# Performance work log

Hardware: AMD Instinct MI355X
Metric: run time of the kernel (lower is better)

Reference implementation:

```python
import jax, jax.numpy as jnp
import numpy as np

B, C, H, W = 64, 256, 32, 32
HID = C // 16          # SE hidden = channels // ratio
EMB = 16               # channel/snr embed dim
COND = 2 * EMB         # cond vector dim = 32
RHID = 64              # rate controller hidden
SNR_DB = 10.0
CH_IDX = 2             # 'Combined_channel'
POWER = 2.0
BASE_CR, MIN_CR, MAX_CR, ALPHA = 0.5, 0.3, 1.0, 0.7


def setup_inputs() -> dict:
    key = jax.random.key(0)
    ks = jax.random.split(key, 16)
    g = lambda k, sh: (jax.random.normal(k, sh, dtype=jnp.float32) * 0.05)
    return {
        "x": jax.random.normal(ks[0], (B, C, H, W), dtype=jnp.float32),
        "channel_embed": g(ks[1], (3, EMB)),
        "snr_w1": g(ks[2], (EMB, 1)), "snr_b1": jnp.zeros((EMB,), jnp.float32),
        "snr_w2": g(ks[3], (EMB, EMB)), "snr_b2": jnp.zeros((EMB,), jnp.float32),
        "base_w1": g(ks[4], (HID, C)),
        "base_w2": g(ks[5], (C, HID)),
        "sem_proj": g(ks[6], (HID, C)),
        "cond_proj": g(ks[7], (HID, COND)),
        "out_proj": g(ks[8], (C, HID)),
        "r_w1": g(ks[9], (RHID, C + COND)), "r_b1": jnp.zeros((RHID,), jnp.float32),
        "r_w2": g(ks[10], (RHID, RHID)), "r_b2": jnp.zeros((RHID,), jnp.float32),
        "r_w3": g(ks[11], (1, RHID)), "r_b3": jnp.zeros((1,), jnp.float32),
    }


def _topk_mask(weights, k):
    # weights [B,C], k [B] int; keep top-k per row (vectorized rank trick).
    order = jnp.argsort(-weights, axis=1)
    ranks = jnp.argsort(order, axis=1)
    return (ranks < k[:, None]).astype(weights.dtype)


def reference(x, channel_embed, snr_w1, snr_b1, snr_w2, snr_b2,
              base_w1, base_w2, sem_proj, cond_proj, out_proj,
              r_w1, r_b1, r_w2, r_b2, r_w3, r_b3):
    b, c, h, w = x.shape
    sem = x.mean(axis=(2, 3))                                   # [B,C] GAP
    # channel condition encoder
    ch_vec = jnp.broadcast_to(channel_embed[CH_IDX], (b, EMB))
    s_in = jnp.full((b, 1), SNR_DB / 28.0, dtype=x.dtype)
    sv = jax.nn.relu(s_in @ snr_w1.T + snr_b1)
    sv = jax.nn.relu(sv @ snr_w2.T + snr_b2)
    cond = jnp.concatenate([ch_vec, sv], axis=1)                # [B,32]
    # base SE weights * channel-conditioned gate
    base = jax.nn.sigmoid(jax.nn.relu(sem @ base_w1.T) @ base_w2.T)
    gate = jax.nn.sigmoid(jax.nn.relu(sem @ sem_proj.T + cond @ cond_proj.T) @ out_proj.T)
    weights = base * gate                                       # [B,C]
    # rate controller -> per-sample cr
    r = jax.nn.relu(jnp.concatenate([sem, cond], axis=1) @ r_w1.T + r_b1)
    r = jax.nn.relu(r @ r_w2.T + r_b2)
    raw = jax.nn.sigmoid(r @ r_w3.T + r_b3)[:, 0]
    dyn = MIN_CR + (MAX_CR - MIN_CR) * raw
    cr = jnp.clip((1.0 - ALPHA) * BASE_CR + ALPHA * dyn, MIN_CR, MAX_CR)
    k = jnp.clip(jnp.round(cr * c).astype(jnp.int32), 1, c)
    mask = _topk_mask(weights, k)
    z = x * (weights * mask)[:, :, None, None]                  # masked latent
    # --- combined channel: flat Rayleigh fading + per-(b,c,h) AWGN ---
    F = c * h * w
    zf = z.reshape(b, F)
    xr, xi = zf[:, 0::2], zf[:, 1::2]                           # [B,F/2]
    nk = jax.random.split(jax.random.key(42), 5)
    hr = jax.random.normal(nk[0], xr.shape, x.dtype)            # torch h_i (real)
    hi = jax.random.normal(nk[1], xr.shape, x.dtype)            # torch h_r (imag)
    std = jnp.sqrt(jnp.asarray(POWER / (10.0 ** (SNR_DB / 10.0)), x.dtype))
    nr = std * jax.random.normal(nk[2], xr.shape, x.dtype)
    ni = std * jax.random.normal(nk[3], xr.shape, x.dtype)
    yr = hr * xr - hi * xi + nr
    yi = hr * xi + hi * xr + ni
    den = hr * hr + hi * hi
    outr = (yr * hr + yi * hi) / den
    outi = (yi * hr - yr * hi) / den
    faded = jnp.stack([outr, outi], axis=-1).reshape(b, c, h, w)
    # per-(b,c,h) random SNR map AWGN
    kk = jax.random.split(nk[4], 2)
    snr_map = jax.random.randint(kk[0], (b, c, h, 1), 0, 29).astype(x.dtype)
    std2 = jnp.sqrt(POWER / (10.0 ** (snr_map / 10.0)))
    return faded + std2 * jax.random.normal(kk[1], (b, c, h, w), x.dtype)
```

## Files before the change

### kernel.cpp

```cpp
#include <hip/hip_runtime.h>

#define NB 64
#define NC 256
#define NF 262144
#define NPAIR 131072
#define NROWS 524288

struct U2 { unsigned a, b; };

__host__ __device__ constexpr unsigned rotl32(unsigned x, int d) {
  return (x << d) | (x >> (32 - d));
}

__host__ __device__ constexpr U2 tf2x32(unsigned k0, unsigned k1,
                                        unsigned x0, unsigned x1) {
  const unsigned ks0 = k0, ks1 = k1, ks2 = k0 ^ k1 ^ 0x1BD11BDAu;
  x0 += ks0; x1 += ks1;
  x0 += x1; x1 = rotl32(x1, 13); x1 ^= x0;
  x0 += x1; x1 = rotl32(x1, 15); x1 ^= x0;
  x0 += x1; x1 = rotl32(x1, 26); x1 ^= x0;
  x0 += x1; x1 = rotl32(x1, 6);  x1 ^= x0;
  x0 += ks1; x1 += ks2 + 1u;
  x0 += x1; x1 = rotl32(x1, 17); x1 ^= x0;
  x0 += x1; x1 = rotl32(x1, 29); x1 ^= x0;
  x0 += x1; x1 = rotl32(x1, 16); x1 ^= x0;
  x0 += x1; x1 = rotl32(x1, 24); x1 ^= x0;
  x0 += ks2; x1 += ks0 + 2u;
  x0 += x1; x1 = rotl32(x1, 13); x1 ^= x0;
  x0 += x1; x1 = rotl32(x1, 15); x1 ^= x0;
  x0 += x1; x1 = rotl32(x1, 26); x1 ^= x0;
  x0 += x1; x1 = rotl32(x1, 6);  x1 ^= x0;
  x0 += ks0; x1 += ks1 + 3u;
  x0 += x1; x1 = rotl32(x1, 17); x1 ^= x0;
  x0 += x1; x1 = rotl32(x1, 29); x1 ^= x0;
  x0 += x1; x1 = rotl32(x1, 16); x1 ^= x0;
  x0 += x1; x1 = rotl32(x1, 24); x1 ^= x0;
  x0 += ks1; x1 += ks2 + 4u;
  x0 += x1; x1 = rotl32(x1, 13); x1 ^= x0;
  x0 += x1; x1 = rotl32(x1, 15); x1 ^= x0;
  x0 += x1; x1 = rotl32(x1, 26); x1 ^= x0;
  x0 += x1; x1 = rotl32(x1, 6);  x1 ^= x0;
  x0 += ks2; x1 += ks0 + 5u;
  return U2{x0, x1};
}

constexpr U2 NK0 = tf2x32(0u, 42u, 0u, 0u);
constexpr U2 NK1 = tf2x32(0u, 42u, 0u, 1u);
constexpr U2 NK2 = tf2x32(0u, 42u, 0u, 2u);
constexpr U2 NK3 = tf2x32(0u, 42u, 0u, 3u);
constexpr U2 NK4 = tf2x32(0u, 42u, 0u, 4u);
constexpr U2 KK0 = tf2x32(NK4.a, NK4.b, 0u, 0u);
constexpr U2 KK1 = tf2x32(NK4.a, NK4.b, 0u, 1u);

__device__ __forceinline__ unsigned rb32(unsigned k0, unsigned k1, unsigned m) {
  const unsigned ks2 = k0 ^ k1 ^ 0x1BD11BDAu;
  unsigned x0 = k0, x1 = m + k1;
#define QR(r) x0 += x1; x1 = __builtin_rotateleft32(x1, r); x1 ^= x0;
  QR(13) QR(15) QR(26) QR(6)
  x0 += k1;  x1 += ks2 + 1u;
  QR(17) QR(29) QR(16) QR(24)
  x0 += ks2; x1 += k0 + 2u;
  QR(13) QR(15) QR(26) QR(6)
  x0 += k0;  x1 += k1 + 3u;
  QR(17) QR(29) QR(16) QR(24)
  x0 += k1;  x1 += ks2 + 4u;
  QR(13) QR(15) QR(26) QR(6)
  x0 += ks2; x1 += k0 + 5u;
#undef QR
  return x0 ^ x1;
}

__device__ __forceinline__ float normal_fast(unsigned bits) {
  const float lo = __uint_as_float(0xBF7FFFFFu);
  float u = __uint_as_float((bits >> 9) | 0x3F800000u) - 1.0f;
  float v = fmaf(u, 2.0f, lo);
  float t = fmaf(-v, v, 1.0f);
  float w = __builtin_amdgcn_logf(t) * -0.69314718f;
  float p;
  if (w < 5.0f) {
    float z = w - 2.5f;
    p = 2.81022636e-08f;
    p = fmaf(p, z, 3.43273939e-07f);
    p = fmaf(p, z, -3.5233877e-06f);
    p = fmaf(p, z, -4.39150654e-06f);
    p = fmaf(p, z, 0.00021858087f);
    p = fmaf(p, z, -0.00125372503f);
    p = fmaf(p, z, -0.00417768164f);
    p = fmaf(p, z, 0.246640727f);
    p = fmaf(p, z, 1.50140941f);
  } else {
    float z = __builtin_amdgcn_sqrtf(w) - 3.0f;
    p = -0.000200214257f;
    p = fmaf(p, z, 0.000100950558f);
    p = fmaf(p, z, 0.00134934322f);
    p = fmaf(p, z, -0.00367342844f);
    p = fmaf(p, z, 0.00573950773f);
    p = fmaf(p, z, -0.0076224613f);
    p = fmaf(p, z, 0.00943887047f);
    p = fmaf(p, z, 1.00167406f);
    p = fmaf(p, z, 2.83297682f);
  }
  return 1.41421356f * (p * v);
}

__global__ __launch_bounds__(256) void sem_kernel(const float* __restrict__ x,
                                                  float* __restrict__ sem) {
  int row = (blockIdx.x * 256 + threadIdx.x) >> 6;
  int lane = threadIdx.x & 63;
  const float* rp = x + (size_t)row * 1024;
  float acc = 0.0f;
#pragma unroll
  for (int i = 0; i < 4; ++i) {
    float4 v = *(const float4*)(rp + i * 256 + lane * 4);
    acc += v.x + v.y + v.z + v.w;
  }
#pragma unroll
  for (int off = 32; off > 0; off >>= 1) acc += __shfl_down(acc, off, 64);
  if (lane == 0) sem[row] = acc * (1.0f / 1024.0f);
}

__global__ __launch_bounds__(256) void head_kernel(
    const float* __restrict__ sem_g, const float* __restrict__ channel_embed,
    const float* __restrict__ snr_w1, const float* __restrict__ snr_b1,
    const float* __restrict__ snr_w2, const float* __restrict__ snr_b2,
    const float* __restrict__ base_w1, const float* __restrict__ base_w2,
    const float* __restrict__ sem_proj, const float* __restrict__ cond_proj,
    const float* __restrict__ out_proj, const float* __restrict__ r_w1,
    const float* __restrict__ r_b1, const float* __restrict__ r_w2,
    const float* __restrict__ r_b2, const float* __restrict__ r_w3,
    const float* __restrict__ r_b3, float* __restrict__ s_out) {
  __shared__ float sem_s[256];
  __shared__ float sv1_s[16];
  __shared__ float cond_s[32];
  __shared__ float hid_s[16], g1_s[16];
  __shared__ float r1_s[64], r2_s[64];
  __shared__ float w_s[256];
  __shared__ int k_s;
  const int b = blockIdx.x, t = threadIdx.x;

  sem_s[t] = sem_g[b * 256 + t];
  if (t < 16) {
    const float s_in = (float)(10.0 / 28.0);
    sv1_s[t] = fmaxf(0.0f, s_in * snr_w1[t] + snr_b1[t]);
  }
  __syncthreads();
  if (t < 16) {
    float a = snr_b2[t];
    for (int f = 0; f < 16; ++f) a += sv1_s[f] * snr_w2[t * 16 + f];
    cond_s[16 + t] = fmaxf(0.0f, a);
    cond_s[t] = channel_embed[2 * 16 + t];
  }
  __syncthreads();
  if (t < 16) {
    float a1 = 0.0f, a2 = 0.0f;
    for (int c = 0; c < 256; ++c) {
      float sc = sem_s[c];
      a1 += sc * base_w1[t * 256 + c];
      a2 += sc * sem_proj[t * 256 + c];
    }
    for (int j = 0; j < 32; ++j) a2 += cond_s[j] * cond_proj[t * 32 + j];
    hid_s[t] = fmaxf(0.0f, a1);
    g1_s[t] = fmaxf(0.0f, a2);
  } else if (t < 80) {
    int i = t - 16;
    float a = r_b1[i];
    for (int c = 0; c < 256; ++c) a += sem_s[c] * r_w1[i * 288 + c];
    for (int j = 0; j < 32; ++j) a += cond_s[j] * r_w1[i * 288 + 256 + j];
    r1_s[i] = fmaxf(0.0f, a);
  }
  __syncthreads();
  if (t < 64) {
    float a = r_b2[t];
    for (int j = 0; j < 64; ++j) a += r1_s[j] * r_w2[t * 64 + j];
    r2_s[t] = fmaxf(0.0f, a);
  }
  {
    float a1 = 0.0f, a2 = 0.0f;
    for (int i = 0; i < 16; ++i) {
      a1 += hid_s[i] * base_w2[t * 16 + i];
      a2 += g1_s[i] * out_proj[t * 16 + i];
    }
    float base = 1.0f / (1.0f + expf(-a1));
    float gate = 1.0f / (1.0f + expf(-a2));
    w_s[t] = base * gate;
  }
  __syncthreads();
  if (t == 0) {
    float a = r_b3[0];
    for (int j = 0; j < 64; ++j) a += r2_s[j] * r_w3[j];
    float raw = 1.0f / (1.0f + expf(-a));
    float dyn = 0.3f + 0.7f * raw;
    float cr = 0.15f + 0.7f * dyn;
    cr = fminf(fmaxf(cr, 0.3f), 1.0f);
    int k = (int)rintf(cr * 256.0f);
    k_s = min(max(k, 1), 256);
  }
  __syncthreads();
  {
    float wc = w_s[t];
    int cnt = 0;
    for (int j = 0; j < 256; ++j) {
      float wj = w_s[j];
      cnt += (wj > wc) || (wj == wc && j < t);
    }
    s_out[b * 256 + t] = (cnt < k_s) ? wc : 0.0f;
  }
}

__global__ __launch_bounds__(256) void sim_kernel(const float* __restrict__ x,
                                                  const float* __restrict__ s,
                                                  float* __restrict__ out) {
  const unsigned tid = blockIdx.x * 256u + threadIdx.x;
  const unsigned q0 = tid * 4u;
  const unsigned lane = threadIdx.x & 63u;

  const unsigned wavebase = blockIdx.x * 256u + (threadIdx.x & ~63u);
  const unsigned R0 = wavebase >> 3;
  unsigned su = rb32(KK0.a, KK0.b,
                     ((lane & 8u) ? NROWS : 0u) + R0 + (lane & 7u));
  const unsigned g = lane >> 3;
  unsigned hb = __shfl(su, (int)g, 64);
  unsigned lb = __shfl(su, (int)(8u + g), 64);
  unsigned snr = ((hb % 29u) * 16u + (lb % 29u)) % 29u;
  float std2 = __builtin_amdgcn_sqrtf(
      2.0f * __builtin_amdgcn_exp2f((float)snr * -0.33219281f));

  const unsigned m0 = tid * 2u, m1 = m0 + 1u;
  float hr0 = normal_fast(rb32(NK0.a, NK0.b, m0));
  float hr1 = normal_fast(rb32(NK0.a, NK0.b, m1));
  float hi0 = normal_fast(rb32(NK1.a, NK1.b, m0));
  float hi1 = normal_fast(rb32(NK1.a, NK1.b, m1));
  const float STD = 0.44721359f;
  float nr0 = STD * normal_fast(rb32(NK2.a, NK2.b, m0));
  float nr1 = STD * normal_fast(rb32(NK2.a, NK2.b, m1));
  float ni0 = STD * normal_fast(rb32(NK3.a, NK3.b, m0));
  float ni1 = STD * normal_fast(rb32(NK3.a, NK3.b, m1));
  float n20 = normal_fast(rb32(KK1.a, KK1.b, q0));
  float n21 = normal_fast(rb32(KK1.a, KK1.b, q0 + 1u));
  float n22 = normal_fast(rb32(KK1.a, KK1.b, q0 + 2u));
  float n23 = normal_fast(rb32(KK1.a, KK1.b, q0 + 3u));

  const float4 xv = *(const float4*)(x + q0);
  const float sc = s[q0 >> 10];
  const float xr0 = xv.x * sc, xi0 = xv.y * sc;
  const float xr1 = xv.z * sc, xi1 = xv.w * sc;

  const float den0 = fmaf(hr0, hr0, hi0 * hi0);
  const float den1 = fmaf(hr1, hr1, hi1 * hi1);
  const float rc0 = __builtin_amdgcn_rcpf(den0);
  const float rc1 = __builtin_amdgcn_rcpf(den1);
  const float outr0 = fmaf(fmaf(hr0, nr0, hi0 * ni0), rc0, xr0);
  const float outi0 = fmaf(fmaf(hr0, ni0, -(hi0 * nr0)), rc0, xi0);
  const float outr1 = fmaf(fmaf(hr1, nr1, hi1 * ni1), rc1, xr1);
  const float outi1 = fmaf(fmaf(hr1, ni1, -(hi1 * nr1)), rc1, xi1);

  float4 o;
  o.x = fmaf(std2, n20, outr0);
  o.y = fmaf(std2, n21, outi0);
  o.z = fmaf(std2, n22, outr1);
  o.w = fmaf(std2, n23, outi1);
  *(float4*)(out + q0) = o;
}

extern "C" void kernel_launch(void* const* d_in, const int* in_sizes, int n_in,
                              void* d_out, int out_size, void* d_ws,
                              size_t ws_size, hipStream_t stream) {
  const float* x = (const float*)d_in[0];
  const float* channel_embed = (const float*)d_in[1];
  const float* snr_w1 = (const float*)d_in[2];
  const float* snr_b1 = (const float*)d_in[3];
  const float* snr_w2 = (const float*)d_in[4];
  const float* snr_b2 = (const float*)d_in[5];
  const float* base_w1 = (const float*)d_in[6];
  const float* base_w2 = (const float*)d_in[7];
  const float* sem_proj = (const float*)d_in[8];
  const float* cond_proj = (const float*)d_in[9];
  const float* out_proj = (const float*)d_in[10];
  const float* r_w1 = (const float*)d_in[11];
  const float* r_b1 = (const float*)d_in[12];
  const float* r_w2 = (const float*)d_in[13];
  const float* r_b2 = (const float*)d_in[14];
  const float* r_w3 = (const float*)d_in[15];
  const float* r_b3 = (const float*)d_in[16];

  float* sem = (float*)d_ws;
  float* s = sem + NB * NC;

  sem_kernel<<<NB * NC / 4, 256, 0, stream>>>(x, sem);
  head_kernel<<<NB, 256, 0, stream>>>(sem, channel_embed, snr_w1, snr_b1,
                                      snr_w2, snr_b2, base_w1, base_w2,
                                      sem_proj, cond_proj, out_proj, r_w1,
                                      r_b1, r_w2, r_b2, r_w3, r_b3, s);
  sim_kernel<<<NB * NPAIR / 2 / 256, 256, 0, stream>>>(x, s, (float*)d_out);
}
```

Baseline: 138.6 us.

## Precompute per-row SNR noise std in separate kernel and widen sim work per thread

Moves the per-(b,c,h) random SNR std computation out of the main simulation kernel into a dedicated kernel that writes one std value per row to workspace. The sim kernel then reads that value instead of running threefry and wave shuffles. Each thread now handles 8 outputs instead of 4, with two float4 loads and stores, to amortize per-thread overhead. This costs an extra launch, 2 MB of workspace traffic, and higher register pressure per thread, which may reduce occupancy.

```diff
diff --git a/kernel.cpp b/kernel.cpp
--- a/kernel.cpp
+++ b/kernel.cpp
@@ -103,6 +103,15 @@
   return 1.41421356f * (p * v);
 }
 
+__global__ __launch_bounds__(256) void snr_kernel(float* __restrict__ std2) {
+  const unsigned j = blockIdx.x * 256u + threadIdx.x;
+  unsigned hb = rb32(KK0.a, KK0.b, j);
+  unsigned lb = rb32(KK0.a, KK0.b, NROWS + j);
+  unsigned snr = ((hb % 29u) * 16u + (lb % 29u)) % 29u;
+  std2[j] = __builtin_amdgcn_sqrtf(
+      2.0f * __builtin_amdgcn_exp2f((float)snr * -0.33219281f));
+}
+
 __global__ __launch_bounds__(256) void sem_kernel(const float* __restrict__ x,
                                                   float* __restrict__ sem) {
   int row = (blockIdx.x * 256 + threadIdx.x) >> 6;
@@ -209,57 +218,53 @@
 
 __global__ __launch_bounds__(256) void sim_kernel(const float* __restrict__ x,
                                                   const float* __restrict__ s,
+                                                  const float* __restrict__ std2v,
                                                   float* __restrict__ out) {
   const unsigned tid = blockIdx.x * 256u + threadIdx.x;
-  const unsigned q0 = tid * 4u;
-  const unsigned lane = threadIdx.x & 63u;
-
-  const unsigned wavebase = blockIdx.x * 256u + (threadIdx.x & ~63u);
-  const unsigned R0 = wavebase >> 3;
-  unsigned su = rb32(KK0.a, KK0.b,
-                     ((lane & 8u) ? NROWS : 0u) + R0 + (lane & 7u));
-  const unsigned g = lane >> 3;
-  unsigned hb = __shfl(su, (int)g, 64);
-  unsigned lb = __shfl(su, (int)(8u + g), 64);
-  unsigned snr = ((hb % 29u) * 16u + (lb % 29u)) % 29u;
-  float std2 = __builtin_amdgcn_sqrtf(
-      2.0f * __builtin_amdgcn_exp2f((float)snr * -0.33219281f));
-
-  const unsigned m0 = tid * 2u, m1 = m0 + 1u;
-  float hr0 = normal_fast(rb32(NK0.a, NK0.b, m0));
-  float hr1 = normal_fast(rb32(NK0.a, NK0.b, m1));
-  float hi0 = normal_fast(rb32(NK1.a, NK1.b, m0));
-  float hi1 = normal_fast(rb32(NK1.a, NK1.b, m1));
+  const unsigned q0 = tid * 8u;
+
+  const float4 xa = *(const float4*)(x + q0);
+  const float4 xb = *(const float4*)(x + q0 + 4);
+  const float sc = s[q0 >> 10];
+  const float std2 = std2v[q0 >> 5];
+
+  const unsigned m0 = tid * 4u;
+  float hr[4], hi[4], nr[4], ni[4], n2[8];
   const float STD = 0.44721359f;
-  float nr0 = STD * normal_fast(rb32(NK2.a, NK2.b, m0));
-  float nr1 = STD * normal_fast(rb32(NK2.a, NK2.b, m1));
-  float ni0 = STD * normal_fast(rb32(NK3.a, NK3.b, m0));
-  float ni1 = STD * normal_fast(rb32(NK3.a, NK3.b, m1));
-  float n20 = normal_fast(rb32(KK1.a, KK1.b, q0));
-  float n21 = normal_fast(rb32(KK1.a, KK1.b, q0 + 1u));
-  float n22 = normal_fast(rb32(KK1.a, KK1.b, q0 + 2u));
-  float n23 = normal_fast(rb32(KK1.a, KK1.b, q0 + 3u));
-
-  const float4 xv = *(const float4*)(x + q0);
-  const float sc = s[q0 >> 10];
-  const float xr0 = xv.x * sc, xi0 = xv.y * sc;
-  const float xr1 = xv.z * sc, xi1 = xv.w * sc;
-
-  const float den0 = fmaf(hr0, hr0, hi0 * hi0);
-  const float den1 = fmaf(hr1, hr1, hi1 * hi1);
-  const float rc0 = __builtin_amdgcn_rcpf(den0);
-  const float rc1 = __builtin_amdgcn_rcpf(den1);
-  const float outr0 = fmaf(fmaf(hr0, nr0, hi0 * ni0), rc0, xr0);
-  const float outi0 = fmaf(fmaf(hr0, ni0, -(hi0 * nr0)), rc0, xi0);
-  const float outr1 = fmaf(fmaf(hr1, nr1, hi1 * ni1), rc1, xr1);
-  const float outi1 = fmaf(fmaf(hr1, ni1, -(hi1 * nr1)), rc1, xi1);
-
-  float4 o;
-  o.x = fmaf(std2, n20, outr0);
-  o.y = fmaf(std2, n21, outi0);
-  o.z = fmaf(std2, n22, outr1);
-  o.w = fmaf(std2, n23, outi1);
-  *(float4*)(out + q0) = o;
+#pragma unroll
+  for (int i = 0; i < 4; ++i) hr[i] = normal_fast(rb32(NK0.a, NK0.b, m0 + i));
+#pragma unroll
+  for (int i = 0; i < 4; ++i) hi[i] = normal_fast(rb32(NK1.a, NK1.b, m0 + i));
+#pragma unroll
+  for (int i = 0; i < 4; ++i)
+    nr[i] = STD * normal_fast(rb32(NK2.a, NK2.b, m0 + i));
+#pragma unroll
+  for (int i = 0; i < 4; ++i)
+    ni[i] = STD * normal_fast(rb32(NK3.a, NK3.b, m0 + i));
+#pragma unroll
+  for (int i = 0; i < 8; ++i) n2[i] = normal_fast(rb32(KK1.a, KK1.b, q0 + i));
+
+  float xs[8] = {xa.x * sc, xa.y * sc, xa.z * sc, xa.w * sc,
+                 xb.x * sc, xb.y * sc, xb.z * sc, xb.w * sc};
+  float o[8];
+#pragma unroll
+  for (int i = 0; i < 4; ++i) {
+    const float den = fmaf(hr[i], hr[i], hi[i] * hi[i]);
+    const float rc = __builtin_amdgcn_rcpf(den);
+    o[2 * i] = fmaf(fmaf(hr[i], nr[i], hi[i] * ni[i]), rc, xs[2 * i]);
+    o[2 * i + 1] = fmaf(fmaf(hr[i], ni[i], -(hi[i] * nr[i])), rc, xs[2 * i + 1]);
+  }
+  float4 oa, ob;
+  oa.x = fmaf(std2, n2[0], o[0]);
+  oa.y = fmaf(std2, n2[1], o[1]);
+  oa.z = fmaf(std2, n2[2], o[2]);
+  oa.w = fmaf(std2, n2[3], o[3]);
+  ob.x = fmaf(std2, n2[4], o[4]);
+  ob.y = fmaf(std2, n2[5], o[5]);
+  ob.z = fmaf(std2, n2[6], o[6]);
+  ob.w = fmaf(std2, n2[7], o[7]);
+  *(float4*)(out + q0) = oa;
+  *(float4*)(out + q0 + 4) = ob;
 }
 
 extern "C" void kernel_launch(void* const* d_in, const int* in_sizes, int n_in,
@@ -283,13 +288,15 @@
   const float* r_w3 = (const float*)d_in[15];
   const float* r_b3 = (const float*)d_in[16];
 
-  float* sem = (float*)d_ws;
+  float* std2 = (float*)d_ws;
+  float* sem = std2 + NROWS;
   float* s = sem + NB * NC;
 
   sem_kernel<<<NB * NC / 4, 256, 0, stream>>>(x, sem);
+  snr_kernel<<<NROWS / 256, 256, 0, stream>>>(std2);
   head_kernel<<<NB, 256, 0, stream>>>(sem, channel_embed, snr_w1, snr_b1,
                                       snr_w2, snr_b2, base_w1, base_w2,
                                       sem_proj, cond_proj, out_proj, r_w1,
                                       r_b1, r_w2, r_b2, r_w3, r_b3, s);
-  sim_kernel<<<NB * NPAIR / 2 / 256, 256, 0, stream>>>(x, s, (float*)d_out);
-}
+  sim_kernel<<<NB * NF / 8 / 256, 256, 0, stream>>>(x, s, std2, (float*)d_out);
+}
```

Result: faster. 134.3 us (-3.1%).
